# Kernel optimization log

Measured on AMD Instinct MI355X. Metric: run time of the kernel, lower is better.

Reference implementation:

```python
import jax, jax.numpy as jnp
import numpy as np

N_NODES = 4096
N_EDGES = 131072
NUM_USERS = 50000
NUM_ITEMS = 50000
EMB = 64
NUM_CLASSES = 41476
BN_EPS = 1e-5


def _seg_sum(x, idx, n):
    return jax.ops.segment_sum(x, idx, num_segments=n)


def gcn_conv(x, ei, W, b):
    # PyG GCNConv: linear, add self-loops, sym norm D^-1/2 (A+I) D^-1/2, sum-agg, +bias
    n = x.shape[0]
    h = x @ W
    loop = jnp.arange(n, dtype=ei.dtype)
    row = jnp.concatenate([ei[0], loop])
    col = jnp.concatenate([ei[1], loop])
    deg = _seg_sum(jnp.ones_like(col, h.dtype), col, n)
    dinv = jnp.where(deg > 0, deg ** -0.5, 0.0)
    norm = dinv[row] * dinv[col]
    return _seg_sum(h[row] * norm[:, None], col, n) + b


def sage_conv(x, ei, Wl, bl, Wr):
    # PyG SAGEConv (mean aggr): mean_neighbors(x) @ Wl + bl + x @ Wr
    n = x.shape[0]
    ones = jnp.ones((ei.shape[1],), x.dtype)
    cnt = _seg_sum(ones, ei[1], n)
    agg = _seg_sum(x[ei[0]], ei[1], n) / jnp.maximum(cnt, 1.0)[:, None]
    return agg @ Wl + bl + x @ Wr


def cheb_conv(x, ei, W0, W1, b):
    # PyG ChebConv K=2, sym norm, lambda_max=2: L_hat = L - I = -D^-1/2 A D^-1/2
    # out = x @ W0 + (L_hat x) @ W1 + b
    n = x.shape[0]
    ones = jnp.ones((ei.shape[1],), x.dtype)
    deg = _seg_sum(ones, ei[0], n)  # row-sum degree (get_laplacian)
    dinv = jnp.where(deg > 0, deg ** -0.5, 0.0)
    w = -(dinv[ei[0]] * dinv[ei[1]])
    tx1 = _seg_sum(x[ei[0]] * w[:, None], ei[1], n)
    return x @ W0 + tx1 @ W1 + b


def gat_conv(x, ei, W, a_src, a_dst, b):
    # PyG GATConv heads=1, concat=False, self-loops added, leaky_relu(0.2) + softmax over in-edges
    n = x.shape[0]
    h = x @ W
    loop = jnp.arange(n, dtype=ei.dtype)
    row = jnp.concatenate([ei[0], loop])
    col = jnp.concatenate([ei[1], loop])
    a_s = h @ a_src  # [n]
    a_d = h @ a_dst
    e = jax.nn.leaky_relu(a_s[row] + a_d[col], 0.2)
    emax = jax.ops.segment_max(e, col, num_segments=n)  # every segment nonempty (self-loops)
    ex = jnp.exp(e - emax[col])
    denom = _seg_sum(ex, col, n)
    alpha = ex / denom[col]
    return _seg_sum(h[row] * alpha[:, None], col, n) + b


def batch_norm(x, g, be):
    mu = jnp.mean(x, axis=0)
    var = jnp.var(x, axis=0)
    return (x - mu) * jax.lax.rsqrt(var + BN_EPS) * g + be


def setup_inputs() -> dict:
    key = jax.random.key(0)
    ks = iter(jax.random.split(key, 48))
    nrm = lambda shape, s=0.05: jax.random.normal(next(ks), shape, jnp.float32) * s
    edge_index = jax.random.randint(next(ks), (2, N_EDGES), 0, N_NODES, jnp.int32)
    node_x = jax.random.randint(next(ks), (N_NODES, 2), 0, NUM_USERS, jnp.int32)
    inp = dict(
        edge_index=edge_index, node_x=node_x,
        user_emb_w=nrm((NUM_USERS, EMB)), item_emb_w=nrm((NUM_ITEMS, EMB)),
        mlp_w1=nrm((2 * EMB, 1024)), mlp_b1=jnp.zeros((1024,), jnp.float32),
        mlp_w2=nrm((1024, 512)), mlp_b2=jnp.zeros((512,), jnp.float32),
        gcn_w1=nrm((512, 256)), gcn_b1=jnp.zeros((256,), jnp.float32),
        bn1_g=jnp.ones((256,), jnp.float32), bn1_b=jnp.zeros((256,), jnp.float32),
        gcn_w2=nrm((256, 128)), gcn_b2=jnp.zeros((128,), jnp.float32),
        bn2_g=jnp.ones((128,), jnp.float32), bn2_b=jnp.zeros((128,), jnp.float32),
        sage_wl=nrm((128, 128)), sage_bl=jnp.zeros((128,), jnp.float32), sage_wr=nrm((128, 128)),
        cheb_w0=nrm((128, 128)), cheb_w1=nrm((128, 128)), cheb_b=jnp.zeros((128,), jnp.float32),
        gat1_w=nrm((128, 128)), gat1_asrc=nrm((128,)), gat1_adst=nrm((128,)), gat1_b=jnp.zeros((128,), jnp.float32),
        gat2_w=nrm((128, 128)), gat2_asrc=nrm((128,)), gat2_adst=nrm((128,)), gat2_b=jnp.zeros((128,), jnp.float32),
        pred_w=nrm((128, NUM_CLASSES)), pred_b=jnp.zeros((NUM_CLASSES,), jnp.float32),
    )
    return inp


def reference(edge_index, node_x, user_emb_w, item_emb_w, mlp_w1, mlp_b1, mlp_w2, mlp_b2,
              gcn_w1, gcn_b1, bn1_g, bn1_b, gcn_w2, gcn_b2, bn2_g, bn2_b,
              sage_wl, sage_bl, sage_wr, cheb_w0, cheb_w1, cheb_b,
              gat1_w, gat1_asrc, gat1_adst, gat1_b, gat2_w, gat2_asrc, gat2_adst, gat2_b,
              pred_w, pred_b):
    u = user_emb_w[node_x[:, 0]]
    i = item_emb_w[node_x[:, 1]]
    x = jnp.concatenate([u, i], axis=1)  # [N, 2*EMB]
    x = jax.nn.relu(x @ mlp_w1 + mlp_b1)  # dropout = identity (eval mode)
    x = jax.nn.relu(x @ mlp_w2 + mlp_b2)
    x = jax.nn.relu(batch_norm(gcn_conv(x, edge_index, gcn_w1, gcn_b1), bn1_g, bn1_b))
    x = jax.nn.relu(batch_norm(gcn_conv(x, edge_index, gcn_w2, gcn_b2), bn2_g, bn2_b))
    x = jax.nn.relu(sage_conv(x, edge_index, sage_wl, sage_bl, sage_wr))
    x = jax.nn.relu(cheb_conv(x, edge_index, cheb_w0, cheb_w1, cheb_b))
    x = jax.nn.elu(gat_conv(x, edge_index, gat1_w, gat1_asrc, gat1_adst, gat1_b))
    x = jax.nn.elu(gat_conv(x, edge_index, gat2_w, gat2_asrc, gat2_adst, gat2_b))
    return x @ pred_w + pred_b  # [N, NUM_CLASSES]
```

## Files before the change

kernel.cpp:

```cpp
#include <hip/hip_runtime.h>
#include <math.h>

#define NN 4096
#define NE 131072
#define NCLS 41476
#define NPAD 41600

typedef __attribute__((ext_vector_type(8))) unsigned short ushort8;
typedef __attribute__((ext_vector_type(8))) __bf16 bf16x8;
typedef __attribute__((ext_vector_type(4))) float f32x4;

__device__ __forceinline__ unsigned short f2bf(float f) {
  unsigned u = __float_as_uint(f);
  unsigned r = u + 0x7fffu + ((u >> 16) & 1u);
  return (unsigned short)(r >> 16);
}
__device__ __forceinline__ float bf2f(unsigned short u) {
  return __uint_as_float(((unsigned)u) << 16);
}

__global__ void k_gather(const int* __restrict__ node_x, const float* __restrict__ uw,
                         const float* __restrict__ iw, unsigned short* __restrict__ x0) {
  int n = blockIdx.x, t = threadIdx.x;
  int u = node_x[n * 2], it = node_x[n * 2 + 1];
  float v = (t < 64) ? uw[u * 64 + t] : iw[it * 64 + (t - 64)];
  x0[n * 128 + t] = f2bf(v);
}

struct CvtDesc { const float* src; unsigned short* dst; int K, N, ld, koff, tile0, ntx; };
struct CvtArgs { CvtDesc d[11]; };

__global__ void k_cvt_all(CvtArgs a) {
  __shared__ float s[32][33];
  int b = blockIdx.x;
  int di = 0;
#pragma unroll
  for (int i = 1; i < 11; i++)
    if (a.d[i].tile0 <= b) di = i;
  const CvtDesc dd = a.d[di];
  int t = b - dd.tile0;
  int n0 = (t % dd.ntx) * 32, k0 = (t / dd.ntx) * 32;
  int tt = threadIdx.x, c = tt & 31, r8 = tt >> 5;
#pragma unroll
  for (int r = 0; r < 4; r++) {
    int k = k0 + r8 + r * 8, n = n0 + c;
    s[r8 + r * 8][c] = (n < dd.N) ? dd.src[(size_t)k * dd.N + n] : 0.f;
  }
  __syncthreads();
#pragma unroll
  for (int r = 0; r < 4; r++) {
    int n = n0 + r8 + r * 8, k = k0 + c;
    dd.dst[(size_t)n * dd.ld + dd.koff + k] = f2bf(s[c][r8 + r * 8]);
  }
}

template <int OUTBF>
__global__ __launch_bounds__(256) void k_bgemm(const unsigned short* __restrict__ A,
                                               const unsigned short* __restrict__ Bt,
                                               const float* __restrict__ bias,
                                               void* __restrict__ Cv, int N, int K, int relu) {
  __shared__ unsigned short As[128 * 128];
  __shared__ unsigned short Bs[128 * 128];
  int m0 = blockIdx.y * 128;
  int n0 = blockIdx.x * 128;
  int tid = threadIdx.x;
  int wave = tid >> 6, lane = tid & 63;
  int wm = (wave >> 1) * 64, wn = (wave & 1) * 64;
  int lr = lane & 15, lg = lane >> 4;
  f32x4 acc[4][4] = {};
  for (int k0 = 0; k0 < K; k0 += 128) {
#pragma unroll
    for (int i = 0; i < 8; i++) {
      int idx = tid + i * 256;
      int row = idx >> 4, ku = idx & 15;
      int sw = (ku ^ (row & 7)) * 8;
      *reinterpret_cast<ushort8*>(As + row * 128 + sw) =
          *reinterpret_cast<const ushort8*>(A + (size_t)(m0 + row) * K + k0 + ku * 8);
      *reinterpret_cast<ushort8*>(Bs + row * 128 + sw) =
          *reinterpret_cast<const ushort8*>(Bt + (size_t)(n0 + row) * K + k0 + ku * 8);
    }
    __syncthreads();
#pragma unroll
    for (int kk = 0; kk < 4; kk++) {
      bf16x8 af[4], bfr[4];
#pragma unroll
      for (int mi = 0; mi < 4; mi++) {
        int row = wm + mi * 16 + lr;
        af[mi] = __builtin_bit_cast(
            bf16x8, *reinterpret_cast<const ushort8*>(As + row * 128 + (((kk * 4 + lg) ^ (row & 7)) * 8)));
        int col = wn + mi * 16 + lr;
        bfr[mi] = __builtin_bit_cast(
            bf16x8, *reinterpret_cast<const ushort8*>(Bs + col * 128 + (((kk * 4 + lg) ^ (col & 7)) * 8)));
      }
#pragma unroll
      for (int mi = 0; mi < 4; mi++)
#pragma unroll
        for (int ni = 0; ni < 4; ni++)
          acc[mi][ni] = __builtin_amdgcn_mfma_f32_16x16x32_bf16(af[mi], bfr[ni], acc[mi][ni], 0, 0, 0);
    }
    __syncthreads();
  }
#pragma unroll
  for (int mi = 0; mi < 4; mi++) {
#pragma unroll
    for (int ni = 0; ni < 4; ni++) {
      int col = n0 + wn + ni * 16 + lr;
      if (col < N) {
        float bv = bias ? bias[col] : 0.f;
#pragma unroll
        for (int r = 0; r < 4; r++) {
          int row = m0 + wm + mi * 16 + lg * 4 + r;
          float v = acc[mi][ni][r] + bv;
          if (relu) v = fmaxf(v, 0.f);
          if (OUTBF)
            ((unsigned short*)Cv)[(size_t)row * N + col] = f2bf(v);
          else
            ((float*)Cv)[(size_t)row * N + col] = v;
        }
      }
    }
  }
}

__global__ __launch_bounds__(256) void k_pred_gemm(const unsigned short* __restrict__ A,
                                                   const unsigned short* __restrict__ Bt,
                                                   const float* __restrict__ bias,
                                                   float* __restrict__ C) {
  __shared__ unsigned short As[128 * 128];
  __shared__ unsigned short Bs[128 * 128];
  int n0 = blockIdx.x * 128;
  int tid = threadIdx.x;
  int wave = tid >> 6, lane = tid & 63;
  int wm = (wave >> 1) * 64, wn = (wave & 1) * 64;
  int lr = lane & 15, lg = lane >> 4;
#pragma unroll
  for (int i = 0; i < 8; i++) {
    int idx = tid + i * 256;
    int row = idx >> 4, ku = idx & 15;
    int sw = (ku ^ (row & 7)) * 8;
    *reinterpret_cast<ushort8*>(Bs + row * 128 + sw) =
        *reinterpret_cast<const ushort8*>(Bt + (size_t)(n0 + row) * 128 + ku * 8);
  }
  float bv[4];
  int colv[4];
#pragma unroll
  for (int ni = 0; ni < 4; ni++) {
    colv[ni] = n0 + wn + ni * 16 + lr;
    bv[ni] = (colv[ni] < NCLS) ? bias[colv[ni]] : 0.f;
  }
  int mt0 = blockIdx.y * 16;
  for (int mt = mt0; mt < mt0 + 16; ++mt) {
    int m0 = mt * 128;
    __syncthreads();
#pragma unroll
    for (int i = 0; i < 8; i++) {
      int idx = tid + i * 256;
      int row = idx >> 4, ku = idx & 15;
      int sw = (ku ^ (row & 7)) * 8;
      *reinterpret_cast<ushort8*>(As + row * 128 + sw) =
          *reinterpret_cast<const ushort8*>(A + (size_t)(m0 + row) * 128 + ku * 8);
    }
    __syncthreads();
    f32x4 acc[4][4] = {};
#pragma unroll
    for (int kk = 0; kk < 4; kk++) {
      bf16x8 af[4], bfr[4];
#pragma unroll
      for (int mi = 0; mi < 4; mi++) {
        int row = wm + mi * 16 + lr;
        af[mi] = __builtin_bit_cast(
            bf16x8, *reinterpret_cast<const ushort8*>(As + row * 128 + (((kk * 4 + lg) ^ (row & 7)) * 8)));
        int col = wn + mi * 16 + lr;
        bfr[mi] = __builtin_bit_cast(
            bf16x8, *reinterpret_cast<const ushort8*>(Bs + col * 128 + (((kk * 4 + lg) ^ (col & 7)) * 8)));
      }
#pragma unroll
      for (int mi = 0; mi < 4; mi++)
#pragma unroll
        for (int ni = 0; ni < 4; ni++)
          acc[mi][ni] = __builtin_amdgcn_mfma_f32_16x16x32_bf16(af[mi], bfr[ni], acc[mi][ni], 0, 0, 0);
    }
#pragma unroll
    for (int mi = 0; mi < 4; mi++) {
#pragma unroll
      for (int ni = 0; ni < 4; ni++) {
        if (colv[ni] < NCLS) {
#pragma unroll
          for (int r = 0; r < 4; r++) {
            int row = m0 + wm + mi * 16 + lg * 4 + r;
            C[(size_t)row * NCLS + colv[ni]] = acc[mi][ni][r] + bv[ni];
          }
        }
      }
    }
  }
}

template <int MODE>
__global__ __launch_bounds__(256) void k_bgemm_s(const void* __restrict__ Av,
                                                 const unsigned short* __restrict__ Bt,
                                                 const float* __restrict__ bias,
                                                 unsigned short* __restrict__ C, int ldC,
                                                 int K, int relu,
                                                 const float* __restrict__ scale,
                                                 const float* __restrict__ shift,
                                                 const float* __restrict__ asrc,
                                                 const float* __restrict__ adst,
                                                 float* __restrict__ o_as,
                                                 float* __restrict__ o_ad) {
  __shared__ unsigned short As[32 * 64];
  __shared__ unsigned short Bs[128 * 64];
  __shared__ float sc[256], sh[256];
  __shared__ float sas[4][32], sad[4][32];
  int m0 = blockIdx.y * 32;
  int n0 = blockIdx.x * 128;
  int tid = threadIdx.x;
  int wave = tid >> 6, lane = tid & 63;
  int wn = wave * 32;
  int lr = lane & 15, lg = lane >> 4;
  if (MODE == 1) {
    if (tid < K) { sc[tid] = scale[tid]; sh[tid] = shift[tid]; }
    __syncthreads();
  }
  f32x4 acc[2][2] = {};
  for (int k0 = 0; k0 < K; k0 += 64) {
    {
      int row = tid >> 3, uu = tid & 7, sw = (uu ^ (row & 7)) * 8;
      if (MODE == 1) {
        const float* Af = (const float*)Av;
        const float* p = Af + (size_t)(m0 + row) * K + k0 + uu * 8;
        float4 p0 = *reinterpret_cast<const float4*>(p);
        float4 p1 = *reinterpret_cast<const float4*>(p + 4);
        int kb = k0 + uu * 8;
        float pv[8] = {p0.x, p0.y, p0.z, p0.w, p1.x, p1.y, p1.z, p1.w};
        ushort8 o;
#pragma unroll
        for (int j = 0; j < 8; j++) o[j] = f2bf(fmaxf(pv[j] * sc[kb + j] + sh[kb + j], 0.f));
        *reinterpret_cast<ushort8*>(As + row * 64 + sw) = o;
      } else {
        *reinterpret_cast<ushort8*>(As + row * 64 + sw) =
            *reinterpret_cast<const ushort8*>((const unsigned short*)Av + (size_t)(m0 + row) * K + k0 + uu * 8);
      }
    }
#pragma unroll
    for (int i = 0; i < 4; i++) {
      int idx = tid + i * 256;
      int row = idx >> 3, uu = idx & 7, sw = (uu ^ (row & 7)) * 8;
      *reinterpret_cast<ushort8*>(Bs + row * 64 + sw) =
          *reinterpret_cast<const ushort8*>(Bt + (size_t)(n0 + row) * K + k0 + uu * 8);
    }
    __syncthreads();
#pragma unroll
    for (int kk = 0; kk < 2; kk++) {
      bf16x8 af[2], bfr[2];
#pragma unroll
      for (int mi = 0; mi < 2; mi++) {
        int row = mi * 16 + lr;
        af[mi] = __builtin_bit_cast(
            bf16x8, *reinterpret_cast<const ushort8*>(As + row * 64 + (((kk * 4 + lg) ^ (row & 7)) * 8)));
        int col = wn + mi * 16 + lr;
        bfr[mi] = __builtin_bit_cast(
            bf16x8, *reinterpret_cast<const ushort8*>(Bs + col * 64 + (((kk * 4 + lg) ^ (col & 7)) * 8)));
      }
#pragma unroll
      for (int mi = 0; mi < 2; mi++)
#pragma unroll
        for (int ni = 0; ni < 2; ni++)
          acc[mi][ni] = __builtin_amdgcn_mfma_f32_16x16x32_bf16(af[mi], bfr[ni], acc[mi][ni], 0, 0, 0);
    }
    __syncthreads();
  }
  float dss[2][4] = {}, dsd[2][4] = {};
#pragma unroll
  for (int mi = 0; mi < 2; mi++) {
#pragma unroll
    for (int ni = 0; ni < 2; ni++) {
      int col = n0 + wn + ni * 16 + lr;
      float bv = bias ? bias[col] : 0.f;
      float ac = (MODE == 2) ? asrc[col] : 0.f;
      float dc = (MODE == 2) ? adst[col] : 0.f;
#pragma unroll
      for (int r = 0; r < 4; r++) {
        int row = m0 + mi * 16 + lg * 4 + r;
        float v = acc[mi][ni][r] + bv;
        if (relu) v = fmaxf(v, 0.f);
        C[(size_t)row * ldC + col] = f2bf(v);
        if (MODE == 2) { dss[mi][r] += v * ac; dsd[mi][r] += v * dc; }
      }
    }
  }
  if (MODE == 2) {
#pragma unroll
    for (int mi = 0; mi < 2; mi++)
#pragma unroll
      for (int r = 0; r < 4; r++) {
#pragma unroll
        for (int mask = 1; mask < 16; mask <<= 1) {
          dss[mi][r] += __shfl_xor(dss[mi][r], mask);
          dsd[mi][r] += __shfl_xor(dsd[mi][r], mask);
        }
        if (lr == 0) {
          int rowloc = mi * 16 + lg * 4 + r;
          sas[wave][rowloc] = dss[mi][r];
          sad[wave][rowloc] = dsd[mi][r];
        }
      }
    __syncthreads();
    if (tid < 32) {
      float s = sas[0][tid] + sas[1][tid] + sas[2][tid] + sas[3][tid];
      float d = sad[0][tid] + sad[1][tid] + sad[2][tid] + sad[3][tid];
      o_as[m0 + tid] = s;
      o_ad[m0 + tid] = d;
    }
  }
}

__global__ void k_count2(const int* __restrict__ ei, int* __restrict__ deg0,
                         int* __restrict__ deg1) {
  for (int i = blockIdx.x * blockDim.x + threadIdx.x; i < 2 * NE; i += gridDim.x * blockDim.x) {
    int v = ei[i];
    atomicAdd((i < NE ? deg0 : deg1) + v, 1);
  }
}

__global__ void k_scan4096(const int* __restrict__ deg1, const int* __restrict__ deg0,
                           int* __restrict__ rowptr, int* __restrict__ cursor,
                           float* __restrict__ dinvA, float* __restrict__ dinv0) {
  __shared__ int s[1024];
  int t = threadIdx.x;
  int4 d = *reinterpret_cast<const int4*>(deg1 + t * 4);
  float4 dv = {rsqrtf((float)(d.x + 1)), rsqrtf((float)(d.y + 1)),
               rsqrtf((float)(d.z + 1)), rsqrtf((float)(d.w + 1))};
  *reinterpret_cast<float4*>(dinvA + t * 4) = dv;
  int4 d0 = *reinterpret_cast<const int4*>(deg0 + t * 4);
  float4 dv0 = {d0.x > 0 ? rsqrtf((float)d0.x) : 0.f, d0.y > 0 ? rsqrtf((float)d0.y) : 0.f,
                d0.z > 0 ? rsqrtf((float)d0.z) : 0.f, d0.w > 0 ? rsqrtf((float)d0.w) : 0.f};
  *reinterpret_cast<float4*>(dinv0 + t * 4) = dv0;
  int sum = d.x + d.y + d.z + d.w;
  s[t] = sum;
  __syncthreads();
  for (int off = 1; off < 1024; off <<= 1) {
    int x = (t >= off) ? s[t - off] : 0;
    __syncthreads();
    s[t] += x;
    __syncthreads();
  }
  int base = s[t] - sum;
  int4 o;
  o.x = base; o.y = base + d.x; o.z = o.y + d.y; o.w = o.z + d.z;
  *reinterpret_cast<int4*>(rowptr + t * 4) = o;
  *reinterpret_cast<int4*>(cursor + t * 4) = o;
  if (t == 1023) rowptr[4096] = base + sum;
}

__global__ void k_fill(const int* __restrict__ ei0, const int* __restrict__ ei1,
                       int* __restrict__ cursor, int* __restrict__ csr_src) {
  int e = blockIdx.x * blockDim.x + threadIdx.x;
  if (e < NE) {
    int pos = atomicAdd(&cursor[ei1[e]], 1);
    csr_src[pos] = ei0[e];
  }
}

template <int VEC>
__global__ void k_gcn_agg(const unsigned short* __restrict__ h, const int* __restrict__ rowptr,
                          const int* __restrict__ csr_src, const float* __restrict__ dinv,
                          float* __restrict__ out) {
  constexpr int F = 64 * VEC;
  __shared__ int sld[128];
  __shared__ float wld[128];
  __shared__ float red[3][64 * VEC];
  int c = blockIdx.x, tid = threadIdx.x, wv = tid >> 6, ln = tid & 63;
  float dc = dinv[c];
  int r0 = rowptr[c], r1 = rowptr[c + 1];
  float acc[VEC] = {};
  for (int base = r0; base < r1; base += 128) {
    int nb = min(128, r1 - base);
    __syncthreads();
    if (tid < nb) { int s = csr_src[base + tid]; sld[tid] = s; wld[tid] = dinv[s]; }
    __syncthreads();
    for (int i = wv; i < nb; i += 4) {
      float w = wld[i];
      const unsigned short* p = h + (size_t)sld[i] * F + ln * VEC;
      if (VEC == 2) {
        ushort2 v = *reinterpret_cast<const ushort2*>(p);
        acc[0] += bf2f(v.x) * w; acc[1] += bf2f(v.y) * w;
      } else {
        ushort4 v = *reinterpret_cast<const ushort4*>(p);
        acc[0] += bf2f(v.x) * w; acc[1] += bf2f(v.y) * w;
        acc[2] += bf2f(v.z) * w; acc[3] += bf2f(v.w) * w;
      }
    }
  }
  if (wv) {
#pragma unroll
    for (int j = 0; j < VEC; j++) red[wv - 1][ln * VEC + j] = acc[j];
  }
  __syncthreads();
  if (wv == 0) {
    const unsigned short* pc = h + (size_t)c * F + ln * VEC;
#pragma unroll
    for (int j = 0; j < VEC; j++) {
      acc[j] += red[0][ln * VEC + j] + red[1][ln * VEC + j] + red[2][ln * VEC + j];
      acc[j] += bf2f(pc[j]) * dc;
      out[(size_t)c * F + ln * VEC + j] = acc[j] * dc;
    }
  }
}

__global__ void k_sage_agg(const unsigned short* __restrict__ x, const int* __restrict__ rowptr,
                           const int* __restrict__ csr_src, unsigned short* __restrict__ out) {
  __shared__ int sld[128];
  __shared__ float red[3][128];
  int c = blockIdx.x, tid = threadIdx.x, wv = tid >> 6, ln = tid & 63;
  int r0 = rowptr[c], r1 = rowptr[c + 1];
  float a0 = 0.f, a1 = 0.f;
  for (int base = r0; base < r1; base += 128) {
    int nb = min(128, r1 - base);
    __syncthreads();
    if (tid < nb) sld[tid] = csr_src[base + tid];
    __syncthreads();
    for (int i = wv; i < nb; i += 4) {
      ushort2 v = *reinterpret_cast<const ushort2*>(x + (size_t)sld[i] * 256 + ln * 2);
      a0 += bf2f(v.x); a1 += bf2f(v.y);
    }
  }
  if (wv) { red[wv - 1][ln * 2] = a0; red[wv - 1][ln * 2 + 1] = a1; }
  __syncthreads();
  if (wv == 0) {
    a0 += red[0][ln * 2] + red[1][ln * 2] + red[2][ln * 2];
    a1 += red[0][ln * 2 + 1] + red[1][ln * 2 + 1] + red[2][ln * 2 + 1];
    float inv = 1.f / fmaxf((float)(r1 - r0), 1.f);
    ushort2 o; o.x = f2bf(a0 * inv); o.y = f2bf(a1 * inv);
    *reinterpret_cast<ushort2*>(out + (size_t)c * 256 + ln * 2) = o;
  }
}

__global__ void k_cheb_agg(const unsigned short* __restrict__ x, const int* __restrict__ rowptr,
                           const int* __restrict__ csr_src, const float* __restrict__ dinv0,
                           unsigned short* __restrict__ out) {
  __shared__ int sld[128];
  __shared__ float wld[128];
  __shared__ float red[3][128];
  int c = blockIdx.x, tid = threadIdx.x, wv = tid >> 6, ln = tid & 63;
  int r0 = rowptr[c], r1 = rowptr[c + 1];
  float a0 = 0.f, a1 = 0.f;
  for (int base = r0; base < r1; base += 128) {
    int nb = min(128, r1 - base);
    __syncthreads();
    if (tid < nb) { int s = csr_src[base + tid]; sld[tid] = s; wld[tid] = dinv0[s]; }
    __syncthreads();
    for (int i = wv; i < nb; i += 4) {
      float w = wld[i];
      ushort2 v = *reinterpret_cast<const ushort2*>(x + (size_t)sld[i] * 256 + ln * 2);
      a0 += bf2f(v.x) * w; a1 += bf2f(v.y) * w;
    }
  }
  if (wv) { red[wv - 1][ln * 2] = a0; red[wv - 1][ln * 2 + 1] = a1; }
  __syncthreads();
  if (wv == 0) {
    a0 += red[0][ln * 2] + red[1][ln * 2] + red[2][ln * 2];
    a1 += red[0][ln * 2 + 1] + red[1][ln * 2 + 1] + red[2][ln * 2 + 1];
    float s = -dinv0[c];
    ushort2 o; o.x = f2bf(a0 * s); o.y = f2bf(a1 * s);
    *reinterpret_cast<ushort2*>(out + (size_t)c * 256 + ln * 2) = o;
  }
}

__global__ void k_gat_agg(const unsigned short* __restrict__ h, const int* __restrict__ rowptr,
                          const int* __restrict__ csr_src, const float* __restrict__ a_s,
                          const float* __restrict__ a_d, const float* __restrict__ bias,
                          unsigned short* __restrict__ out) {
  __shared__ int sld[128];
  __shared__ float eld[128];
  __shared__ float red[3][128];
  __shared__ float sden[4];
  __shared__ float smax[256];
  int c = blockIdx.x, tid = threadIdx.x, wv = tid >> 6, ln = tid & 63;
  int r0 = rowptr[c], r1 = rowptr[c + 1];
  float adc = a_d[c];
  float es = a_s[c] + adc;
  es = es >= 0.f ? es : 0.2f * es;
  float m = es;
  for (int i = r0 + tid; i < r1; i += 256) {
    float v = a_s[csr_src[i]] + adc;
    m = fmaxf(m, v >= 0.f ? v : 0.2f * v);
  }
  smax[tid] = m;
  __syncthreads();
  for (int sft = 128; sft; sft >>= 1) {
    if (tid < sft) smax[tid] = fmaxf(smax[tid], smax[tid + sft]);
    __syncthreads();
  }
  m = smax[0];
  float a0 = 0.f, a1 = 0.f, den = 0.f;
  for (int base = r0; base < r1; base += 128) {
    int nb = min(128, r1 - base);
    __syncthreads();
    if (tid < nb) {
      int s = csr_src[base + tid];
      sld[tid] = s;
      float v = a_s[s] + adc;
      v = v >= 0.f ? v : 0.2f * v;
      eld[tid] = expf(v - m);
    }
    __syncthreads();
    for (int i = wv; i < nb; i += 4) {
      float w = eld[i];
      den += w;
      ushort2 v = *reinterpret_cast<const ushort2*>(h + (size_t)sld[i] * 128 + ln * 2);
      a0 += w * bf2f(v.x); a1 += w * bf2f(v.y);
    }
  }
  if (wv) {
    red[wv - 1][ln * 2] = a0; red[wv - 1][ln * 2 + 1] = a1;
    if (ln == 0) sden[wv] = den;
  }
  __syncthreads();
  if (wv == 0) {
    a0 += red[0][ln * 2] + red[1][ln * 2] + red[2][ln * 2];
    a1 += red[0][ln * 2 + 1] + red[1][ln * 2 + 1] + red[2][ln * 2 + 1];
    den += sden[1] + sden[2] + sden[3];
    float ws = expf(es - m);
    den += ws;
    ushort2 xc = *reinterpret_cast<const ushort2*>(h + (size_t)c * 128 + ln * 2);
    a0 += ws * bf2f(xc.x); a1 += ws * bf2f(xc.y);
    float inv = 1.f / den;
    float v0 = a0 * inv + bias[ln * 2];
    float v1 = a1 * inv + bias[ln * 2 + 1];
    v0 = v0 > 0.f ? v0 : expm1f(v0);
    v1 = v1 > 0.f ? v1 : expm1f(v1);
    ushort2 o; o.x = f2bf(v0); o.y = f2bf(v1);
    *reinterpret_cast<ushort2*>(out + (size_t)c * 128 + ln * 2) = o;
  }
}

__global__ void k_bn_stats(const float* __restrict__ x, float* __restrict__ psum,
                           float* __restrict__ psq, int F) {
  int tid = threadIdx.x;
  int f = tid & (F - 1);
  int rstep = 256 / F;
  int r0 = tid / F;
  int base = blockIdx.x * 64;
  float s = 0.f, s2 = 0.f;
  for (int rr = r0; rr < 64; rr += rstep) {
    float v = x[(size_t)(base + rr) * F + f];
    s += v;
    s2 += v * v;
  }
  int slot = blockIdx.x * rstep + r0;
  psum[(size_t)slot * F + f] = s;
  psq[(size_t)slot * F + f] = s2;
}

__global__ void k_bn_final(const float* __restrict__ psum, const float* __restrict__ psq,
                           const float* __restrict__ g, const float* __restrict__ be,
                           float* __restrict__ scale, float* __restrict__ shift, int F) {
  int f = threadIdx.x;
  int S = 16384 / F;
  float s = 0.f, s2 = 0.f;
  for (int i = 0; i < S; i++) {
    s += psum[(size_t)i * F + f];
    s2 += psq[(size_t)i * F + f];
  }
  float invM = 1.f / (float)NN;
  float mu = s * invM;
  float var = s2 * invM - mu * mu;
  float sc = g[f] * rsqrtf(var + 1e-5f);
  scale[f] = sc;
  shift[f] = be[f] - mu * sc;
}

__global__ void k_bn_apply(const float* __restrict__ x, const float* __restrict__ scale,
                           const float* __restrict__ shift, unsigned short* __restrict__ y,
                           int ldY, int logF, int n) {
  int F1 = (1 << logF) - 1;
  for (int i = blockIdx.x * blockDim.x + threadIdx.x; i < n; i += gridDim.x * blockDim.x) {
    int row = i >> logF, f = i & F1;
    float v = fmaxf(x[i] * scale[f] + shift[f], 0.f);
    y[(size_t)row * ldY + f] = f2bf(v);
  }
}

static inline int cdiv(int a, int b) { return (a + b - 1) / b; }

extern "C" void kernel_launch(void* const* d_in, const int* in_sizes, int n_in,
                              void* d_out, int out_size, void* d_ws, size_t ws_size,
                              hipStream_t stream) {
  const int* ei = (const int*)d_in[0];
  const int* ei0 = ei;
  const int* ei1 = ei + NE;
  const int* node_x = (const int*)d_in[1];
  const float* user_w = (const float*)d_in[2];
  const float* item_w = (const float*)d_in[3];
  const float* mlp_w1 = (const float*)d_in[4];
  const float* mlp_b1 = (const float*)d_in[5];
  const float* mlp_w2 = (const float*)d_in[6];
  const float* mlp_b2 = (const float*)d_in[7];
  const float* gcn_w1 = (const float*)d_in[8];
  const float* bn1_g = (const float*)d_in[10];
  const float* bn1_b = (const float*)d_in[11];
  const float* gcn_w2 = (const float*)d_in[12];
  const float* bn2_g = (const float*)d_in[14];
  const float* bn2_b = (const float*)d_in[15];
  const float* sage_wl = (const float*)d_in[16];
  const float* sage_bl = (const float*)d_in[17];
  const float* sage_wr = (const float*)d_in[18];
  const float* cheb_w0 = (const float*)d_in[19];
  const float* cheb_w1 = (const float*)d_in[20];
  const float* cheb_b = (const float*)d_in[21];
  const float* gat1_w = (const float*)d_in[22];
  const float* gat1_as = (const float*)d_in[23];
  const float* gat1_ad = (const float*)d_in[24];
  const float* gat1_b = (const float*)d_in[25];
  const float* gat2_w = (const float*)d_in[26];
  const float* gat2_as = (const float*)d_in[27];
  const float* gat2_ad = (const float*)d_in[28];
  const float* gat2_b = (const float*)d_in[29];
  const float* pred_w = (const float*)d_in[30];
  const float* pred_b = (const float*)d_in[31];

  char* w = (char*)d_ws;
  size_t off = 0;
  auto alloc = [&](size_t bytes) -> char* {
    char* p = w + off;
    off = (off + bytes + 255) & ~(size_t)255;
    return p;
  };
  unsigned short* x0b = (unsigned short*)alloc((size_t)NN * 128 * 2);
  unsigned short* x1b = (unsigned short*)alloc((size_t)NN * 1024 * 2);
  unsigned short* x2b = (unsigned short*)alloc((size_t)NN * 512 * 2);
  unsigned short* h1b = (unsigned short*)alloc((size_t)NN * 256 * 2);
  unsigned short* catS = (unsigned short*)alloc((size_t)NN * 256 * 2);
  unsigned short* catC = (unsigned short*)alloc((size_t)NN * 256 * 2);
  unsigned short* xb2 = (unsigned short*)alloc((size_t)NN * 128 * 2);
  unsigned short* hb = (unsigned short*)alloc((size_t)NN * 128 * 2);
  unsigned short* xa2 = (unsigned short*)alloc((size_t)NN * 128 * 2);
  unsigned short* xb3 = (unsigned short*)alloc((size_t)NN * 128 * 2);
  float* agg = (float*)alloc((size_t)NN * 256 * 4);
  unsigned short* w1t = (unsigned short*)alloc((size_t)1024 * 128 * 2);
  unsigned short* w2t = (unsigned short*)alloc((size_t)512 * 1024 * 2);
  unsigned short* g1t = (unsigned short*)alloc((size_t)256 * 512 * 2);
  unsigned short* g2t = (unsigned short*)alloc((size_t)128 * 256 * 2);
  unsigned short* sgt = (unsigned short*)alloc((size_t)128 * 256 * 2);
  unsigned short* cht = (unsigned short*)alloc((size_t)128 * 256 * 2);
  unsigned short* a1t = (unsigned short*)alloc((size_t)128 * 128 * 2);
  unsigned short* a2t = (unsigned short*)alloc((size_t)128 * 128 * 2);
  unsigned short* predT = (unsigned short*)alloc((size_t)NPAD * 128 * 2);
  int* deg0 = (int*)alloc(NN * 4);
  int* deg1 = (int*)alloc(NN * 4);
  int* rowptr = (int*)alloc((NN + 1) * 4);
  int* cursor = (int*)alloc(NN * 4);
  int* csr_src = (int*)alloc(NE * 4);
  float* dinvA = (float*)alloc(NN * 4);
  float* dinv0 = (float*)alloc(NN * 4);
  float* a_s = (float*)alloc(NN * 4);
  float* a_d = (float*)alloc(NN * 4);
  float* psum = (float*)alloc(16384 * 4);
  float* psq = (float*)alloc(16384 * 4);
  float* bscale = (float*)alloc(256 * 4);
  float* bshift = (float*)alloc(256 * 4);

  CvtArgs ca;
  int t0 = 0;
  auto mkd = [&](int i, const float* src, unsigned short* dst, int K, int N, int ld, int koff,
                 int ntx) {
    ca.d[i] = {src, dst, K, N, ld, koff, t0, ntx};
    t0 += ntx * (K / 32);
  };
  mkd(0, mlp_w1, w1t, 128, 1024, 128, 0, 32);
  mkd(1, mlp_w2, w2t, 1024, 512, 1024, 0, 16);
  mkd(2, gcn_w1, g1t, 512, 256, 512, 0, 8);
  mkd(3, gcn_w2, g2t, 256, 128, 256, 0, 4);
  mkd(4, sage_wl, sgt, 128, 128, 256, 0, 4);
  mkd(5, sage_wr, sgt, 128, 128, 256, 128, 4);
  mkd(6, cheb_w0, cht, 128, 128, 256, 0, 4);
  mkd(7, cheb_w1, cht, 128, 128, 256, 128, 4);
  mkd(8, gat1_w, a1t, 128, 128, 128, 0, 4);
  mkd(9, gat2_w, a2t, 128, 128, 128, 0, 4);
  mkd(10, pred_w, predT, 128, NCLS, 128, 0, NPAD / 32);
  k_cvt_all<<<t0, 256, 0, stream>>>(ca);

  hipMemsetAsync(deg0, 0, 2 * NN * 4, stream);
  k_count2<<<512, 256, 0, stream>>>(ei, deg0, deg1);
  k_scan4096<<<1, 1024, 0, stream>>>(deg1, deg0, rowptr, cursor, dinvA, dinv0);
  k_fill<<<cdiv(NE, 256), 256, 0, stream>>>(ei0, ei1, cursor, csr_src);

  k_gather<<<NN, 128, 0, stream>>>(node_x, user_w, item_w, x0b);
  k_bgemm<1><<<dim3(8, 32), 256, 0, stream>>>(x0b, w1t, mlp_b1, x1b, 1024, 128, 1);
  k_bgemm<1><<<dim3(4, 32), 256, 0, stream>>>(x1b, w2t, mlp_b2, x2b, 512, 1024, 1);

  k_bgemm_s<0><<<dim3(2, 128), 256, 0, stream>>>(x2b, g1t, nullptr, h1b, 256, 512, 0,
                                                 nullptr, nullptr, nullptr, nullptr, nullptr, nullptr);
  k_gcn_agg<4><<<NN, 256, 0, stream>>>(h1b, rowptr, csr_src, dinvA, agg);
  k_bn_stats<<<64, 256, 0, stream>>>(agg, psum, psq, 256);
  k_bn_final<<<1, 256, 0, stream>>>(psum, psq, bn1_g, bn1_b, bscale, bshift, 256);

  k_bgemm_s<1><<<dim3(1, 128), 256, 0, stream>>>(agg, g2t, nullptr, hb, 128, 256, 0,
                                                 bscale, bshift, nullptr, nullptr, nullptr, nullptr);
  k_gcn_agg<2><<<NN, 256, 0, stream>>>(hb, rowptr, csr_src, dinvA, agg);
  k_bn_stats<<<64, 256, 0, stream>>>(agg, psum, psq, 128);
  k_bn_final<<<1, 128, 0, stream>>>(psum, psq, bn2_g, bn2_b, bscale, bshift, 128);
  k_bn_apply<<<1024, 256, 0, stream>>>(agg, bscale, bshift, catS + 128, 256, 7, NN * 128);

  k_sage_agg<<<NN, 256, 0, stream>>>(catS + 128, rowptr, csr_src, catS);
  k_bgemm_s<0><<<dim3(1, 128), 256, 0, stream>>>(catS, sgt, sage_bl, catC, 256, 256, 1,
                                                 nullptr, nullptr, nullptr, nullptr, nullptr, nullptr);

  k_cheb_agg<<<NN, 256, 0, stream>>>(catC, rowptr, csr_src, dinv0, catC + 128);
  k_bgemm_s<0><<<dim3(1, 128), 256, 0, stream>>>(catC, cht, cheb_b, xb2, 128, 256, 1,
                                                 nullptr, nullptr, nullptr, nullptr, nullptr, nullptr);

  k_bgemm_s<2><<<dim3(1, 128), 256, 0, stream>>>(xb2, a1t, nullptr, hb, 128, 128, 0,
                                                 nullptr, nullptr, gat1_as, gat1_ad, a_s, a_d);
  k_gat_agg<<<NN, 256, 0, stream>>>(hb, rowptr, csr_src, a_s, a_d, gat1_b, xa2);

  k_bgemm_s<2><<<dim3(1, 128), 256, 0, stream>>>(xa2, a2t, nullptr, hb, 128, 128, 0,
                                                 nullptr, nullptr, gat2_as, gat2_ad, a_s, a_d);
  k_gat_agg<<<NN, 256, 0, stream>>>(hb, rowptr, csr_src, a_s, a_d, gat2_b, xb3);

  k_pred_gemm<<<dim3(NPAD / 128, 2), 256, 0, stream>>>(xb3, predT, pred_b, (float*)d_out);
}
```

Before: 494.7 us.

## Fuse setup kernels, fold BN finalize into consumers, double pred GEMM grid

Merges the weight-conversion, degree-count and embedding-gather kernels into one launch that dispatches on block index. BatchNorm finalize is folded into the consuming GEMM prologue and into a new bn_apply kernel, which removes the separate finalize launches and the scale/shift buffers. The prediction GEMM now gives each block 8 row tiles instead of 16, doubling the grid for more parallelism. Every consumer block now redundantly reduces the partial statistics, which adds some duplicated work.

```diff
diff --git a/kernel.cpp b/kernel.cpp
--- a/kernel.cpp
+++ b/kernel.cpp
@@ -19,38 +19,49 @@
   return __uint_as_float(((unsigned)u) << 16);
 }
 
-__global__ void k_gather(const int* __restrict__ node_x, const float* __restrict__ uw,
-                         const float* __restrict__ iw, unsigned short* __restrict__ x0) {
-  int n = blockIdx.x, t = threadIdx.x;
-  int u = node_x[n * 2], it = node_x[n * 2 + 1];
-  float v = (t < 64) ? uw[u * 64 + t] : iw[it * 64 + (t - 64)];
-  x0[n * 128 + t] = f2bf(v);
-}
-
 struct CvtDesc { const float* src; unsigned short* dst; int K, N, ld, koff, tile0, ntx; };
 struct CvtArgs { CvtDesc d[11]; };
 
-__global__ void k_cvt_all(CvtArgs a) {
-  __shared__ float s[32][33];
+__global__ void k_fused0(CvtArgs a, int cvtBlocks, const int* __restrict__ ei,
+                         int* __restrict__ deg0, int* __restrict__ deg1,
+                         const int* __restrict__ node_x, const float* __restrict__ uw,
+                         const float* __restrict__ iw, unsigned short* __restrict__ x0) {
   int b = blockIdx.x;
-  int di = 0;
-#pragma unroll
-  for (int i = 1; i < 11; i++)
-    if (a.d[i].tile0 <= b) di = i;
-  const CvtDesc dd = a.d[di];
-  int t = b - dd.tile0;
-  int n0 = (t % dd.ntx) * 32, k0 = (t / dd.ntx) * 32;
-  int tt = threadIdx.x, c = tt & 31, r8 = tt >> 5;
-#pragma unroll
-  for (int r = 0; r < 4; r++) {
-    int k = k0 + r8 + r * 8, n = n0 + c;
-    s[r8 + r * 8][c] = (n < dd.N) ? dd.src[(size_t)k * dd.N + n] : 0.f;
-  }
-  __syncthreads();
-#pragma unroll
-  for (int r = 0; r < 4; r++) {
-    int n = n0 + r8 + r * 8, k = k0 + c;
-    dd.dst[(size_t)n * dd.ld + dd.koff + k] = f2bf(s[c][r8 + r * 8]);
+  int tid = threadIdx.x;
+  if (b < cvtBlocks) {
+    __shared__ float s[32][33];
+    int di = 0;
+#pragma unroll
+    for (int i = 1; i < 11; i++)
+      if (a.d[i].tile0 <= b) di = i;
+    const CvtDesc dd = a.d[di];
+    int t = b - dd.tile0;
+    int n0 = (t % dd.ntx) * 32, k0 = (t / dd.ntx) * 32;
+    int c = tid & 31, r8 = tid >> 5;
+#pragma unroll
+    for (int r = 0; r < 4; r++) {
+      int k = k0 + r8 + r * 8, n = n0 + c;
+      s[r8 + r * 8][c] = (n < dd.N) ? dd.src[(size_t)k * dd.N + n] : 0.f;
+    }
+    __syncthreads();
+#pragma unroll
+    for (int r = 0; r < 4; r++) {
+      int n = n0 + r8 + r * 8, k = k0 + c;
+      dd.dst[(size_t)n * dd.ld + dd.koff + k] = f2bf(s[c][r8 + r * 8]);
+    }
+  } else if (b < cvtBlocks + 512) {
+    int bid = b - cvtBlocks;
+    for (int i = bid * 256 + tid; i < 2 * NE; i += 512 * 256) {
+      int v = ei[i];
+      atomicAdd((i < NE ? deg0 : deg1) + v, 1);
+    }
+  } else {
+    int nb = b - cvtBlocks - 512;
+    int n = nb * 2 + (tid >> 7);
+    int t = tid & 127;
+    int u = node_x[n * 2], it = node_x[n * 2 + 1];
+    float v = (t < 64) ? uw[u * 64 + t] : iw[it * 64 + (t - 64)];
+    x0[n * 128 + t] = f2bf(v);
   }
 }
 
@@ -148,8 +159,8 @@
     colv[ni] = n0 + wn + ni * 16 + lr;
     bv[ni] = (colv[ni] < NCLS) ? bias[colv[ni]] : 0.f;
   }
-  int mt0 = blockIdx.y * 16;
-  for (int mt = mt0; mt < mt0 + 16; ++mt) {
+  int mt0 = blockIdx.y * 8;
+  for (int mt = mt0; mt < mt0 + 8; ++mt) {
     int m0 = mt * 128;
     __syncthreads();
 #pragma unroll
@@ -202,8 +213,10 @@
                                                  const float* __restrict__ bias,
                                                  unsigned short* __restrict__ C, int ldC,
                                                  int K, int relu,
-                                                 const float* __restrict__ scale,
-                                                 const float* __restrict__ shift,
+                                                 const float* __restrict__ psum,
+                                                 const float* __restrict__ psq,
+                                                 const float* __restrict__ bng,
+                                                 const float* __restrict__ bnb,
                                                  const float* __restrict__ asrc,
                                                  const float* __restrict__ adst,
                                                  float* __restrict__ o_as,
@@ -219,7 +232,20 @@
   int wn = wave * 32;
   int lr = lane & 15, lg = lane >> 4;
   if (MODE == 1) {
-    if (tid < K) { sc[tid] = scale[tid]; sh[tid] = shift[tid]; }
+    if (tid < K) {
+      int S = 16384 / K;
+      float s = 0.f, s2 = 0.f;
+      for (int i = 0; i < S; i++) {
+        s += psum[(size_t)i * K + tid];
+        s2 += psq[(size_t)i * K + tid];
+      }
+      float invM = 1.f / (float)NN;
+      float mu = s * invM;
+      float var = s2 * invM - mu * mu;
+      float scv = bng[tid] * rsqrtf(var + 1e-5f);
+      sc[tid] = scv;
+      sh[tid] = bnb[tid] - mu * scv;
+    }
     __syncthreads();
   }
   f32x4 acc[2][2] = {};
@@ -312,14 +338,6 @@
       o_as[m0 + tid] = s;
       o_ad[m0 + tid] = d;
     }
-  }
-}
-
-__global__ void k_count2(const int* __restrict__ ei, int* __restrict__ deg0,
-                         int* __restrict__ deg1) {
-  for (int i = blockIdx.x * blockDim.x + threadIdx.x; i < 2 * NE; i += gridDim.x * blockDim.x) {
-    int v = ei[i];
-    atomicAdd((i < NE ? deg0 : deg1) + v, 1);
   }
 }
 
@@ -553,31 +571,31 @@
   psq[(size_t)slot * F + f] = s2;
 }
 
-__global__ void k_bn_final(const float* __restrict__ psum, const float* __restrict__ psq,
-                           const float* __restrict__ g, const float* __restrict__ be,
-                           float* __restrict__ scale, float* __restrict__ shift, int F) {
-  int f = threadIdx.x;
-  int S = 16384 / F;
-  float s = 0.f, s2 = 0.f;
-  for (int i = 0; i < S; i++) {
-    s += psum[(size_t)i * F + f];
-    s2 += psq[(size_t)i * F + f];
-  }
-  float invM = 1.f / (float)NN;
-  float mu = s * invM;
-  float var = s2 * invM - mu * mu;
-  float sc = g[f] * rsqrtf(var + 1e-5f);
-  scale[f] = sc;
-  shift[f] = be[f] - mu * sc;
-}
-
-__global__ void k_bn_apply(const float* __restrict__ x, const float* __restrict__ scale,
-                           const float* __restrict__ shift, unsigned short* __restrict__ y,
-                           int ldY, int logF, int n) {
-  int F1 = (1 << logF) - 1;
-  for (int i = blockIdx.x * blockDim.x + threadIdx.x; i < n; i += gridDim.x * blockDim.x) {
-    int row = i >> logF, f = i & F1;
-    float v = fmaxf(x[i] * scale[f] + shift[f], 0.f);
+__global__ void k_bn_apply2(const float* __restrict__ x, const float* __restrict__ psum,
+                            const float* __restrict__ psq, const float* __restrict__ g,
+                            const float* __restrict__ be, unsigned short* __restrict__ y,
+                            int ldY) {
+  __shared__ float sc[128], sh[128];
+  int tid = threadIdx.x;
+  if (tid < 128) {
+    float s = 0.f, s2 = 0.f;
+    for (int i = 0; i < 128; i++) {
+      s += psum[(size_t)i * 128 + tid];
+      s2 += psq[(size_t)i * 128 + tid];
+    }
+    float invM = 1.f / (float)NN;
+    float mu = s * invM;
+    float var = s2 * invM - mu * mu;
+    float scv = g[tid] * rsqrtf(var + 1e-5f);
+    sc[tid] = scv;
+    sh[tid] = be[tid] - mu * scv;
+  }
+  __syncthreads();
+  int f = tid & 127, rhalf = tid >> 7;
+  int row0 = blockIdx.x * 16;
+  for (int rr = 0; rr < 8; rr++) {
+    int row = row0 + rr * 2 + rhalf;
+    float v = fmaxf(x[(size_t)row * 128 + f] * sc[f] + sh[f], 0.f);
     y[(size_t)row * ldY + f] = f2bf(v);
   }
 }
@@ -658,8 +676,6 @@
   float* a_d = (float*)alloc(NN * 4);
   float* psum = (float*)alloc(16384 * 4);
   float* psq = (float*)alloc(16384 * 4);
-  float* bscale = (float*)alloc(256 * 4);
-  float* bshift = (float*)alloc(256 * 4);
 
   CvtArgs ca;
   int t0 = 0;
@@ -679,45 +695,48 @@
   mkd(8, gat1_w, a1t, 128, 128, 128, 0, 4);
   mkd(9, gat2_w, a2t, 128, 128, 128, 0, 4);
   mkd(10, pred_w, predT, 128, NCLS, 128, 0, NPAD / 32);
-  k_cvt_all<<<t0, 256, 0, stream>>>(ca);
 
   hipMemsetAsync(deg0, 0, 2 * NN * 4, stream);
-  k_count2<<<512, 256, 0, stream>>>(ei, deg0, deg1);
+  k_fused0<<<t0 + 512 + NN / 2, 256, 0, stream>>>(ca, t0, ei, deg0, deg1, node_x, user_w,
+                                                  item_w, x0b);
   k_scan4096<<<1, 1024, 0, stream>>>(deg1, deg0, rowptr, cursor, dinvA, dinv0);
   k_fill<<<cdiv(NE, 256), 256, 0, stream>>>(ei0, ei1, cursor, csr_src);
 
-  k_gather<<<NN, 128, 0, stream>>>(node_x, user_w, item_w, x0b);
   k_bgemm<1><<<dim3(8, 32), 256, 0, stream>>>(x0b, w1t, mlp_b1, x1b, 1024, 128, 1);
   k_bgemm<1><<<dim3(4, 32), 256, 0, stream>>>(x1b, w2t, mlp_b2, x2b, 512, 1024, 1);
 
   k_bgemm_s<0><<<dim3(2, 128), 256, 0, stream>>>(x2b, g1t, nullptr, h1b, 256, 512, 0,
-                                                 nullptr, nullptr, nullptr, nullptr, nullptr, nullptr);
+                                                 nullptr, nullptr, nullptr, nullptr, nullptr,
+                                                 nullptr, nullptr, nullptr);
   k_gcn_agg<4><<<NN, 256, 0, stream>>>(h1b, rowptr, csr_src, dinvA, agg);
   k_bn_stats<<<64, 256, 0, stream>>>(agg, psum, psq, 256);
-  k_bn_final<<<1, 256, 0, stream>>>(psum, psq, bn1_g, bn1_b, bscale, bshift, 256);
 
   k_bgemm_s<1><<<dim3(1, 128), 256, 0, stream>>>(agg, g2t, nullptr, hb, 128, 256, 0,
-                                                 bscale, bshift, nullptr, nullptr, nullptr, nullptr);
+                                                 psum, psq, bn1_g, bn1_b, nullptr, nullptr,
+                                                 nullptr, nullptr);
   k_gcn_agg<2><<<NN, 256, 0, stream>>>(hb, rowptr, csr_src, dinvA, agg);
   k_bn_stats<<<64, 256, 0, stream>>>(agg, psum, psq, 128);
-  k_bn_final<<<1, 128, 0, stream>>>(psum, psq, bn2_g, bn2_b, bscale, bshift, 128);
-  k_bn_apply<<<1024, 256, 0, stream>>>(agg, bscale, bshift, catS + 128, 256, 7, NN * 128);
+  k_bn_apply2<<<256, 256, 0, stream>>>(agg, psum, psq, bn2_g, bn2_b, catS + 128, 256);
 
   k_sage_agg<<<NN, 256, 0, stream>>>(catS + 128, rowptr, csr_src, catS);
   k_bgemm_s<0><<<dim3(1, 128), 256, 0, stream>>>(catS, sgt, sage_bl, catC, 256, 256, 1,
-                                                 nullptr, nullptr, nullptr, nullptr, nullptr, nullptr);
+                                                 nullptr, nullptr, nullptr, nullptr, nullptr,
+                                                 nullptr, nullptr, nullptr);
 
   k_cheb_agg<<<NN, 256, 0, stream>>>(catC, rowptr, csr_src, dinv0, catC + 128);
   k_bgemm_s<0><<<dim3(1, 128), 256, 0, stream>>>(catC, cht, cheb_b, xb2, 128, 256, 1,
-                                                 nullptr, nullptr, nullptr, nullptr, nullptr, nullptr);
+                                                 nullptr, nullptr, nullptr, nullptr, nullptr,
+                                                 nullptr, nullptr, nullptr);
 
   k_bgemm_s<2><<<dim3(1, 128), 256, 0, stream>>>(xb2, a1t, nullptr, hb, 128, 128, 0,
-                                                 nullptr, nullptr, gat1_as, gat1_ad, a_s, a_d);
+                                                 nullptr, nullptr, nullptr, nullptr,
+                                                 gat1_as, gat1_ad, a_s, a_d);
   k_gat_agg<<<NN, 256, 0, stream>>>(hb, rowptr, csr_src, a_s, a_d, gat1_b, xa2);
 
   k_bgemm_s<2><<<dim3(1, 128), 256, 0, stream>>>(xa2, a2t, nullptr, hb, 128, 128, 0,
-                                                 nullptr, nullptr, gat2_as, gat2_ad, a_s, a_d);
+                                                 nullptr, nullptr, nullptr, nullptr,
+                                                 gat2_as, gat2_ad, a_s, a_d);
   k_gat_agg<<<NN, 256, 0, stream>>>(hb, rowptr, csr_src, a_s, a_d, gat2_b, xb3);
 
-  k_pred_gemm<<<dim3(NPAD / 128, 2), 256, 0, stream>>>(xb3, predT, pred_b, (float*)d_out);
-}
+  k_pred_gemm<<<dim3(NPAD / 128, 4), 256, 0, stream>>>(xb3, predT, pred_b, (float*)d_out);
+}
```

Measured after the change: 469.9 us. 1.05x faster.
